# Kernel optimization log

Hardware: AMD Instinct MI355X
Metric: run time of the kernel (lower is better)

## Reference

```python
import jax, jax.numpy as jnp
import numpy as np

D_MODEL = 1024
N_HEADS = 16
D_K = D_MODEL // N_HEADS

def _xavier(key, shape):
    fan_in, fan_out = shape[1], shape[0]
    limit = float(np.sqrt(6.0 / (fan_in + fan_out)))
    return jax.random.uniform(key, shape, jnp.float32, -limit, limit)

def setup_inputs() -> dict:
    key = jax.random.key(0)
    ks = jax.random.split(key, 7)
    B, S = 2, 2048
    return {
        "query": jax.random.normal(ks[0], (B, S, D_MODEL), jnp.float32),
        "key": jax.random.normal(ks[1], (B, S, D_MODEL), jnp.float32),
        "value": jax.random.normal(ks[2], (B, S, D_MODEL), jnp.float32),
        "w_q": _xavier(ks[3], (D_MODEL, D_MODEL)),  # torch Linear weight [out, in]
        "w_k": _xavier(ks[4], (D_MODEL, D_MODEL)),
        "w_v": _xavier(ks[5], (D_MODEL, D_MODEL)),
        "w_o": _xavier(ks[6], (D_MODEL, D_MODEL)),
        "ln_gamma": jnp.ones((D_MODEL,), jnp.float32),
        "ln_beta": jnp.zeros((D_MODEL,), jnp.float32),
    }

def reference(query, key, value, w_q, w_k, w_v, w_o, ln_gamma, ln_beta):
    B, S, _ = query.shape
    # projections (torch Linear: x @ W.T), split into heads -> [B, H, S, d_k]
    def split_heads(x, W):
        return (x @ W.T).reshape(B, S, N_HEADS, D_K).transpose(0, 2, 1, 3)
    Q = split_heads(query, w_q)
    K = split_heads(key, w_k)
    V = split_heads(value, w_v)
    scores = jnp.einsum('bhqd,bhkd->bhqk', Q, K) / jnp.sqrt(jnp.float32(D_K))
    attn = jax.nn.softmax(scores, axis=-1)  # dropout disabled (p=0 / eval)
    ctx = jnp.einsum('bhqk,bhkd->bhqd', attn, V)
    ctx = ctx.transpose(0, 2, 1, 3).reshape(B, S, D_MODEL)
    out = ctx @ w_o.T
    # residual + LayerNorm
    x = query + out
    mu = jnp.mean(x, axis=-1, keepdims=True)
    var = jnp.var(x, axis=-1, keepdims=True)
    return (x - mu) / jnp.sqrt(var + 1e-5) * ln_gamma + ln_beta
```

## Files before the change

### kernel.cpp

```cpp
#include <hip/hip_runtime.h>
#include <hip/hip_bf16.h>

#define DEVI __device__ __forceinline__

typedef float f32x4 __attribute__((ext_vector_type(4)));
typedef short bf16x8 __attribute__((ext_vector_type(8)));
typedef unsigned short ushort_t;

DEVI ushort_t f2bf(float x) {
  union { float f; unsigned u; } c; c.f = x;
  unsigned u = c.u;
  unsigned r = (u + 0x7fffu + ((u >> 16) & 1u)) >> 16;
  return (ushort_t)r;
}

DEVI float bf2f(unsigned hw) {
  union { unsigned u; float f; } c; c.u = hw << 16; return c.f;
}

DEVI unsigned cvt_pk_bf16(float lo, float hi) {
  unsigned r;
  asm volatile("v_cvt_pk_bf16_f32 %0, %1, %2" : "=v"(r) : "v"(lo), "v"(hi));
  return r;
}

DEVI void gload16(const ushort_t* g, ushort_t* l) {
  __builtin_amdgcn_global_load_lds(
      (const __attribute__((address_space(1))) unsigned int*)g,
      (__attribute__((address_space(3))) unsigned int*)l, 16, 0, 0);
}

#define WAITL0() asm volatile("s_waitcnt lgkmcnt(0)" ::: "memory")


__global__ __launch_bounds__(256)
void cvt_all_kernel(const float* __restrict__ p0, const float* __restrict__ p1,
                    const float* __restrict__ p2,
                    const float* __restrict__ w0, const float* __restrict__ w1,
                    const float* __restrict__ w2, const float* __restrict__ w3,
                    ushort_t* __restrict__ o0, ushort_t* __restrict__ o1,
                    ushort_t* __restrict__ o2,
                    ushort_t* __restrict__ q0, ushort_t* __restrict__ q1,
                    ushort_t* __restrict__ q2, ushort_t* __restrict__ q3) {
  int z = blockIdx.y;
  int i = blockIdx.x * 256 + threadIdx.x;
  const float* in;
  ushort_t* out;
  if (z < 3) {
    in = (z == 0) ? p0 : (z == 1) ? p1 : p2;
    out = (z == 0) ? o0 : (z == 1) ? o1 : o2;
  } else {
    int w = i >> 17;
    int local = i & 131071;
    in = ((w == 0) ? w0 : (w == 1) ? w1 : (w == 2) ? w2 : w3);
    out = ((w == 0) ? q0 : (w == 1) ? q1 : (w == 2) ? q2 : q3);
    i = local;
  }
  const float4* p = (const float4*)in + (size_t)i * 2;
  float4 a = p[0], b = p[1];
  uint4 v;
  v.x = cvt_pk_bf16(a.x, a.y);
  v.y = cvt_pk_bf16(a.z, a.w);
  v.z = cvt_pk_bf16(b.x, b.y);
  v.w = cvt_pk_bf16(b.z, b.w);
  ((uint4*)out)[i] = v;
}


__global__ __launch_bounds__(256)
void gemm128(const ushort_t* __restrict__ A0, const ushort_t* __restrict__ A1,
             const ushort_t* __restrict__ A2,
             const ushort_t* __restrict__ W0, const ushort_t* __restrict__ W1,
             const ushort_t* __restrict__ W2,
             void* __restrict__ O0, void* __restrict__ O1,
             void* __restrict__ O2, int mode_base, int nsteps, float qscale) {
  constexpr int K = 1024;
  int z = blockIdx.z;
  int mode = (mode_base == 3) ? 3 : mode_base + z;
  const ushort_t* A = (z == 0) ? A0 : (z == 1) ? A1 : A2;
  const ushort_t* W = (z == 0) ? W0 : (z == 1) ? W1 : W2;
  void* Op = (z == 0) ? O0 : (z == 1) ? O1 : O2;
  if (mode == 3) {
    A = A0 + z * 512;
    W = W0 + z * 512;
    Op = z ? O1 : O0;
  }
  float scale = (mode == 0) ? qscale : 1.0f;
  int m0 = (mode == 2) ? blockIdx.x * 128 : blockIdx.y * 128;
  int n0 = (mode == 2) ? blockIdx.y * 128 : blockIdx.x * 128;

  __shared__ __align__(16) ushort_t Asm[2][128 * 64];
  __shared__ __align__(16) ushort_t Bsm[2][128 * 64];

  int t = threadIdx.x;
  int lane = t & 63, wave = t >> 6;
  int wm = wave >> 1, wn = wave & 1;
  int col = lane & 15, g = lane >> 4;
  int lr = lane >> 3, lc = lane & 7;
  int cswz = col & 7;

  const ushort_t* aSrc = A + (size_t)(m0 + wave * 32 + lr) * K + (lc ^ lr) * 8;
  const ushort_t* bSrc = W + (size_t)(n0 + wave * 32 + lr) * K + (lc ^ lr) * 8;

  f32x4 z4 = {0.f, 0.f, 0.f, 0.f};
  f32x4 acc[4][4];
  for (int i = 0; i < 4; i++)
    for (int j = 0; j < 4; j++) acc[i][j] = z4;

#define GEMM_STAGE(buf, koff) do {                                         \
    _Pragma("unroll")                                                      \
    for (int i_ = 0; i_ < 4; i_++) {                                       \
      gload16(aSrc + (koff) + i_ * 8 * K,                                  \
              &Asm[buf][(wave * 32 + i_ * 8) * 64]);                       \
      gload16(bSrc + (koff) + i_ * 8 * K,                                  \
              &Bsm[buf][(wave * 32 + i_ * 8) * 64]);                       \
    }                                                                      \
  } while (0)

  GEMM_STAGE(0, 0);
  __syncthreads();

  for (int kt = 0; kt < nsteps; ++kt) {
    int cur = kt & 1;
    if (kt < nsteps - 1) GEMM_STAGE(cur ^ 1, (kt + 1) * 64);
    const ushort_t* As = Asm[cur];
    const ushort_t* Bs = Bsm[cur];
#pragma unroll
    for (int kk = 0; kk < 2; ++kk) {
      bf16x8 af[4], bfr[4];
#pragma unroll
      for (int mi = 0; mi < 4; mi++) {
        int row = wm * 64 + mi * 16 + col;
        af[mi] = *(const bf16x8*)(As + row * 64 + (((kk * 4 + g) ^ cswz) * 8));
      }
#pragma unroll
      for (int ni = 0; ni < 4; ni++) {
        int row = wn * 64 + ni * 16 + col;
        bfr[ni] = *(const bf16x8*)(Bs + row * 64 + (((kk * 4 + g) ^ cswz) * 8));
      }
      __builtin_amdgcn_s_setprio(1);
#pragma unroll
      for (int mi = 0; mi < 4; mi++)
#pragma unroll
        for (int ni = 0; ni < 4; ni++)
          acc[mi][ni] = __builtin_amdgcn_mfma_f32_16x16x32_bf16(af[mi], bfr[ni],
                                                                acc[mi][ni], 0, 0, 0);
      __builtin_amdgcn_s_setprio(0);
    }
    __syncthreads();
  }

#pragma unroll
  for (int mi = 0; mi < 4; mi++)
#pragma unroll
    for (int ni = 0; ni < 4; ni++)
#pragma unroll
      for (int r = 0; r < 4; r++) {
        int m = m0 + wm * 64 + mi * 16 + g * 4 + r;
        int n = n0 + wn * 64 + ni * 16 + col;
        float v = acc[mi][ni][r] * scale;
        if (mode <= 1) {
          int b = m >> 11, s = m & 2047, h = n >> 6, d = n & 63;
          ((ushort_t*)Op)[(((size_t)(b * 16 + h) * 2048 + s) * 64) + d] = f2bf(v);
        } else if (mode == 2) {
          int h = m >> 6, d = m & 63, b = n >> 11, s = n & 2047;
          ((ushort_t*)Op)[(((size_t)(b * 16 + h) * 64 + d) * 2048) + s] = f2bf(v);
        } else {
          ((ushort_t*)Op)[(size_t)m * 1024 + n] = f2bf(v);
        }
      }
#undef GEMM_STAGE
}


__global__ __launch_bounds__(256, 4)
void attn_kernel(const ushort_t* __restrict__ Qh, const ushort_t* __restrict__ Kh,
                 const ushort_t* __restrict__ Vt,
                 ushort_t* __restrict__ op0, ushort_t* __restrict__ op1,
                 float* __restrict__ lp0, float* __restrict__ lp1) {
  int qt = blockIdx.x;
  int bh = blockIdx.y;
  int sp = blockIdx.z;
  int t = threadIdx.x, lane = t & 63, wave = t >> 6;
  int col = lane & 15, g = lane >> 4;
  int lr = lane >> 3, lc = lane & 7;
  int cswz = col & 7;
  int q0 = qt * 128 + wave * 32;
  int kbase = sp * 1024;
  ushort_t* opart = sp ? op1 : op0;
  float* lpart = sp ? lp1 : lp0;

  const ushort_t* Qp = Qh + (size_t)bh * 2048 * 64;
  const ushort_t* Kp = Kh + (size_t)bh * 2048 * 64;
  const ushort_t* Vp = Vt + (size_t)bh * 64 * 2048;

  __shared__ __align__(16) ushort_t Ksm[2][64 * 64];
  __shared__ __align__(16) ushort_t Vsm[2][64 * 64];

  int slot0 = wave * 16 + lr;
  int slot1 = slot0 + 8;
  int key0 = (slot0 & 0x20) | ((slot0 & 0x0C) << 1) | ((slot0 & 0x10) >> 2) | (slot0 & 3);
  int key1 = (slot1 & 0x20) | ((slot1 & 0x0C) << 1) | ((slot1 & 0x10) >> 2) | (slot1 & 3);

  const ushort_t* kSrc0 = Kp + (size_t)key0 * 64 + (lc ^ lr) * 8;
  const ushort_t* kSrc1 = Kp + (size_t)key1 * 64 + (lc ^ lr) * 8;
  const ushort_t* vSrc = Vp + (size_t)(wave * 16 + lr) * 2048 + (lc ^ lr) * 8;

#define ATTN_STAGE(buf, k0) do { \
    gload16(kSrc0 + (size_t)(k0) * 64, &Ksm[buf][wave * 1024]);        \
    gload16(kSrc1 + (size_t)(k0) * 64, &Ksm[buf][wave * 1024 + 512]);  \
    gload16(vSrc + (k0),               &Vsm[buf][wave * 1024]);        \
    gload16(vSrc + (k0) + 16384,       &Vsm[buf][wave * 1024 + 512]);  \
  } while (0)

  bf16x8 qa0 = *(const bf16x8*)(Qp + (size_t)(q0 + col) * 64 + g * 8);
  bf16x8 qa1 = *(const bf16x8*)(Qp + (size_t)(q0 + col) * 64 + 32 + g * 8);
  bf16x8 qb0 = *(const bf16x8*)(Qp + (size_t)(q0 + 16 + col) * 64 + g * 8);
  bf16x8 qb1 = *(const bf16x8*)(Qp + (size_t)(q0 + 16 + col) * 64 + 32 + g * 8);

  f32x4 z4 = {0.f, 0.f, 0.f, 0.f};
  f32x4 oa[4], ob[4];
  for (int i = 0; i < 4; i++) { oa[i] = z4; ob[i] = z4; }
  f32x4 la = z4, lb = z4;

  ATTN_STAGE(0, kbase);
  __syncthreads();

  for (int it = 0; it < 16; ++it) {
    int cur = it & 1;
    int k0 = kbase + it * 64;
    if (it < 15) ATTN_STAGE(cur ^ 1, k0 + 64);

    const ushort_t* Ks = Ksm[cur];
    const ushort_t* Vs = Vsm[cur];

    f32x4 sa[4], sb[4];
#pragma unroll
    for (int kt = 0; kt < 4; kt++) {
      int off = (kt * 16 + col) * 64 + ((g ^ cswz) * 8);
      bf16x8 kf0 = *(const bf16x8*)(Ks + off);
      bf16x8 kf1 = *(const bf16x8*)(Ks + (off ^ 32));
      f32x4 a = z4, b = z4;
      __builtin_amdgcn_s_setprio(1);
      a = __builtin_amdgcn_mfma_f32_16x16x32_bf16(kf0, qa0, a, 0, 0, 0);
      a = __builtin_amdgcn_mfma_f32_16x16x32_bf16(kf1, qa1, a, 0, 0, 0);
      b = __builtin_amdgcn_mfma_f32_16x16x32_bf16(kf0, qb0, b, 0, 0, 0);
      b = __builtin_amdgcn_mfma_f32_16x16x32_bf16(kf1, qb1, b, 0, 0, 0);
      __builtin_amdgcn_s_setprio(0);
      sa[kt] = a; sb[kt] = b;
    }

    unsigned pka[8], pkb[8];
#pragma unroll
    for (int kt = 0; kt < 4; kt++) {
      float a0 = __builtin_amdgcn_exp2f(sa[kt][0]);
      float a1 = __builtin_amdgcn_exp2f(sa[kt][1]);
      float a2 = __builtin_amdgcn_exp2f(sa[kt][2]);
      float a3 = __builtin_amdgcn_exp2f(sa[kt][3]);
      la[0] += a0; la[1] += a1; la[2] += a2; la[3] += a3;
      pka[2 * kt]     = cvt_pk_bf16(a0, a1);
      pka[2 * kt + 1] = cvt_pk_bf16(a2, a3);
      float b0 = __builtin_amdgcn_exp2f(sb[kt][0]);
      float b1 = __builtin_amdgcn_exp2f(sb[kt][1]);
      float b2 = __builtin_amdgcn_exp2f(sb[kt][2]);
      float b3 = __builtin_amdgcn_exp2f(sb[kt][3]);
      lb[0] += b0; lb[1] += b1; lb[2] += b2; lb[3] += b3;
      pkb[2 * kt]     = cvt_pk_bf16(b0, b1);
      pkb[2 * kt + 1] = cvt_pk_bf16(b2, b3);
    }

#pragma unroll
    for (int kk = 0; kk < 2; kk++) {
      union { uint4 u; bf16x8 f; } ua, ub;
      ua.u.x = pka[4 * kk];     ua.u.y = pka[4 * kk + 1];
      ua.u.z = pka[4 * kk + 2]; ua.u.w = pka[4 * kk + 3];
      ub.u.x = pkb[4 * kk];     ub.u.y = pkb[4 * kk + 1];
      ub.u.z = pkb[4 * kk + 2]; ub.u.w = pkb[4 * kk + 3];
      __builtin_amdgcn_s_setprio(1);
#pragma unroll
      for (int dt = 0; dt < 4; dt++) {
        bf16x8 vf = *(const bf16x8*)(Vs + (dt * 16 + col) * 64 +
                                     (((kk * 4 + g) ^ cswz) * 8));
        oa[dt] = __builtin_amdgcn_mfma_f32_16x16x32_bf16(vf, ua.f, oa[dt], 0, 0, 0);
        ob[dt] = __builtin_amdgcn_mfma_f32_16x16x32_bf16(vf, ub.f, ob[dt], 0, 0, 0);
      }
      __builtin_amdgcn_s_setprio(0);
    }
    __syncthreads();
  }
#undef ATTN_STAGE

  float lva = (la[0] + la[1]) + (la[2] + la[3]);
  lva += __shfl_xor(lva, 16);
  lva += __shfl_xor(lva, 32);
  float lvb = (lb[0] + lb[1]) + (lb[2] + lb[3]);
  lvb += __shfl_xor(lvb, 16);
  lvb += __shfl_xor(lvb, 32);
  if (g == 0) {
    lpart[(size_t)bh * 2048 + q0 + col] = lva;
    lpart[(size_t)bh * 2048 + q0 + 16 + col] = lvb;
  }
  int b = bh >> 4, h = bh & 15;
#pragma unroll
  for (int dt = 0; dt < 4; dt++)
#pragma unroll
    for (int r = 0; r < 4; r++) {
      int d = dt * 16 + g * 4 + r;
      opart[((size_t)(b * 2048 + q0 + col)) * 1024 + h * 64 + d] =
          f2bf(oa[dt][r]);
      opart[((size_t)(b * 2048 + q0 + 16 + col)) * 1024 + h * 64 + d] =
          f2bf(ob[dt][r]);
    }
}


__global__ __launch_bounds__(256)
void attn_reduce(const ushort_t* __restrict__ o0, const ushort_t* __restrict__ o1,
                 const float* __restrict__ l0, const float* __restrict__ l1,
                 ushort_t* __restrict__ ctx) {
  int m = blockIdx.x;
  int t = threadIdx.x;
  int b = m >> 11, q = m & 2047;
  int h = t >> 4;
  size_t li = (size_t)(b * 16 + h) * 2048 + q;
  float inv = 1.0f / (l0[li] + l1[li]);
  uint2 a = ((const uint2*)(o0 + (size_t)m * 1024))[t];
  uint2 c = ((const uint2*)(o1 + (size_t)m * 1024))[t];
  float x0 = (bf2f(a.x & 0xffffu) + bf2f(c.x & 0xffffu)) * inv;
  float x1 = (bf2f(a.x >> 16)     + bf2f(c.x >> 16))     * inv;
  float x2 = (bf2f(a.y & 0xffffu) + bf2f(c.y & 0xffffu)) * inv;
  float x3 = (bf2f(a.y >> 16)     + bf2f(c.y >> 16))     * inv;
  uint2 o;
  o.x = cvt_pk_bf16(x0, x1);
  o.y = cvt_pk_bf16(x2, x3);
  ((uint2*)(ctx + (size_t)m * 1024))[t] = o;
}


__global__ __launch_bounds__(256)
void ln_kernel(const float* __restrict__ resid, const ushort_t* __restrict__ p0,
               const ushort_t* __restrict__ p1,
               const float* __restrict__ gamma, const float* __restrict__ beta,
               float* __restrict__ out) {
  int m = blockIdx.x;
  int t = threadIdx.x;
  int lane = t & 63, wave = t >> 6;
  float4 a = ((const float4*)(resid + (size_t)m * 1024))[t];
  uint2 v0 = ((const uint2*)(p0 + (size_t)m * 1024))[t];
  uint2 v1 = ((const uint2*)(p1 + (size_t)m * 1024))[t];
  float4 x;
  x.x = a.x + bf2f(v0.x & 0xffffu) + bf2f(v1.x & 0xffffu);
  x.y = a.y + bf2f(v0.x >> 16)     + bf2f(v1.x >> 16);
  x.z = a.z + bf2f(v0.y & 0xffffu) + bf2f(v1.y & 0xffffu);
  x.w = a.w + bf2f(v0.y >> 16)     + bf2f(v1.y >> 16);
  float sum = (x.x + x.y) + (x.z + x.w);
  float ssq = x.x * x.x + x.y * x.y + x.z * x.z + x.w * x.w;
  for (int off = 1; off < 64; off <<= 1) {
    sum += __shfl_xor(sum, off);
    ssq += __shfl_xor(ssq, off);
  }
  __shared__ float red[8];
  if (lane == 0) { red[wave] = sum; red[4 + wave] = ssq; }
  __syncthreads();
  sum = red[0] + red[1] + red[2] + red[3];
  ssq = red[4] + red[5] + red[6] + red[7];
  float mu = sum * (1.f / 1024.f);
  float var = ssq * (1.f / 1024.f) - mu * mu;
  float rstd = rsqrtf(var + 1e-5f);
  const float4* gp = (const float4*)gamma;
  const float4* bp = (const float4*)beta;
  float4 gg = gp[t], bb = bp[t];
  float4 y;
  y.x = (x.x - mu) * rstd * gg.x + bb.x;
  y.y = (x.y - mu) * rstd * gg.y + bb.y;
  y.z = (x.z - mu) * rstd * gg.z + bb.z;
  y.w = (x.w - mu) * rstd * gg.w + bb.w;
  ((float4*)(out + (size_t)m * 1024))[t] = y;
}


extern "C" void kernel_launch(void* const* d_in, const int* in_sizes, int n_in,
                              void* d_out, int out_size, void* d_ws, size_t ws_size,
                              hipStream_t stream) {
  (void)in_sizes; (void)n_in; (void)out_size; (void)ws_size;
  const float* query = (const float*)d_in[0];
  const float* keyi  = (const float*)d_in[1];
  const float* value = (const float*)d_in[2];
  const float* w_q = (const float*)d_in[3];
  const float* w_k = (const float*)d_in[4];
  const float* w_v = (const float*)d_in[5];
  const float* w_o = (const float*)d_in[6];
  const float* ln_g = (const float*)d_in[7];
  const float* ln_b = (const float*)d_in[8];

  char* ws = (char*)d_ws;
  const size_t MB = 1u << 20;
  ushort_t* Xq  = (ushort_t*)(ws + 0 * MB);
  ushort_t* Xk  = (ushort_t*)(ws + 8 * MB);
  ushort_t* Xv  = (ushort_t*)(ws + 16 * MB);
  ushort_t* op0 = (ushort_t*)(ws + 0 * MB);
  ushort_t* op1 = (ushort_t*)(ws + 8 * MB);
  float*    l0  = (float*)   (ws + 16 * MB);
  float*    l1  = (float*)   (ws + 17 * MB);
  ushort_t* proj0 = (ushort_t*)(ws + 0 * MB);
  ushort_t* proj1 = (ushort_t*)(ws + 8 * MB);
  ushort_t* Wq  = (ushort_t*)(ws + 24 * MB);
  ushort_t* Wk  = (ushort_t*)(ws + 26 * MB);
  ushort_t* Wv  = (ushort_t*)(ws + 28 * MB);
  ushort_t* Wo  = (ushort_t*)(ws + 30 * MB);
  ushort_t* Qh  = (ushort_t*)(ws + 32 * MB);
  ushort_t* Kh  = (ushort_t*)(ws + 40 * MB);
  ushort_t* Vt  = (ushort_t*)(ws + 48 * MB);
  ushort_t* ctx = (ushort_t*)(ws + 56 * MB);

  const float SCL = 0.18033688f;

  cvt_all_kernel<<<dim3(2048, 4), 256, 0, stream>>>(
      query, keyi, value, w_q, w_k, w_v, w_o,
      Xq, Xk, Xv, Wq, Wk, Wv, Wo);

  gemm128<<<dim3(8, 32, 3), 256, 0, stream>>>(Xq, Xk, Wv, Wq, Wk, Xv,
                                              Qh, Kh, Vt, 0, 16, SCL);
  attn_kernel<<<dim3(16, 32, 2), 256, 0, stream>>>(Qh, Kh, Vt,
                                                   op0, op1, l0, l1);
  attn_reduce<<<4096, 256, 0, stream>>>(op0, op1, l0, l1, ctx);
  gemm128<<<dim3(8, 32, 2), 256, 0, stream>>>(ctx, ctx, ctx, Wo, Wo, Wo,
                                              proj0, proj1, proj0, 3, 8, 1.0f);
  ln_kernel<<<4096, 256, 0, stream>>>(query, proj0, proj1, ln_g, ln_b,
                                      (float*)d_out);
}
```

Baseline: 140.8 us.

## Single-buffer GEMM LDS tiles and swap grid axes for tile rasterization

The projection GEMM drops its double-buffered LDS prefetch. Each k-step now loads its tile, synchronizes, then computes, which halves shared memory per block so more blocks can be resident. The launch grid is also transposed, so consecutive blocks walk along the M (token) dimension instead of N, which changes L2 reuse of the weight and activation tiles. The cost is that global-to-LDS loads no longer overlap with the MFMA work inside a block, and the kernel now relies on other resident blocks to hide that latency.

```diff
diff --git a/kernel.cpp b/kernel.cpp
--- a/kernel.cpp
+++ b/kernel.cpp
@@ -86,11 +86,11 @@
     Op = z ? O1 : O0;
   }
   float scale = (mode == 0) ? qscale : 1.0f;
-  int m0 = (mode == 2) ? blockIdx.x * 128 : blockIdx.y * 128;
-  int n0 = (mode == 2) ? blockIdx.y * 128 : blockIdx.x * 128;
-
-  __shared__ __align__(16) ushort_t Asm[2][128 * 64];
-  __shared__ __align__(16) ushort_t Bsm[2][128 * 64];
+  int m0 = (mode == 2) ? blockIdx.y * 128 : blockIdx.x * 128;
+  int n0 = (mode == 2) ? blockIdx.x * 128 : blockIdx.y * 128;
+
+  __shared__ __align__(16) ushort_t Asm[128 * 64];
+  __shared__ __align__(16) ushort_t Bsm[128 * 64];
 
   int t = threadIdx.x;
   int lane = t & 63, wave = t >> 6;
@@ -107,36 +107,26 @@
   for (int i = 0; i < 4; i++)
     for (int j = 0; j < 4; j++) acc[i][j] = z4;
 
-#define GEMM_STAGE(buf, koff) do {                                         \
-    _Pragma("unroll")                                                      \
-    for (int i_ = 0; i_ < 4; i_++) {                                       \
-      gload16(aSrc + (koff) + i_ * 8 * K,                                  \
-              &Asm[buf][(wave * 32 + i_ * 8) * 64]);                       \
-      gload16(bSrc + (koff) + i_ * 8 * K,                                  \
-              &Bsm[buf][(wave * 32 + i_ * 8) * 64]);                       \
-    }                                                                      \
-  } while (0)
-
-  GEMM_STAGE(0, 0);
-  __syncthreads();
-
   for (int kt = 0; kt < nsteps; ++kt) {
-    int cur = kt & 1;
-    if (kt < nsteps - 1) GEMM_STAGE(cur ^ 1, (kt + 1) * 64);
-    const ushort_t* As = Asm[cur];
-    const ushort_t* Bs = Bsm[cur];
+    int koff = kt * 64;
+#pragma unroll
+    for (int i_ = 0; i_ < 4; i_++) {
+      gload16(aSrc + koff + i_ * 8 * K, &Asm[(wave * 32 + i_ * 8) * 64]);
+      gload16(bSrc + koff + i_ * 8 * K, &Bsm[(wave * 32 + i_ * 8) * 64]);
+    }
+    __syncthreads();
 #pragma unroll
     for (int kk = 0; kk < 2; ++kk) {
       bf16x8 af[4], bfr[4];
 #pragma unroll
       for (int mi = 0; mi < 4; mi++) {
         int row = wm * 64 + mi * 16 + col;
-        af[mi] = *(const bf16x8*)(As + row * 64 + (((kk * 4 + g) ^ cswz) * 8));
+        af[mi] = *(const bf16x8*)(Asm + row * 64 + (((kk * 4 + g) ^ cswz) * 8));
       }
 #pragma unroll
       for (int ni = 0; ni < 4; ni++) {
         int row = wn * 64 + ni * 16 + col;
-        bfr[ni] = *(const bf16x8*)(Bs + row * 64 + (((kk * 4 + g) ^ cswz) * 8));
+        bfr[ni] = *(const bf16x8*)(Bsm + row * 64 + (((kk * 4 + g) ^ cswz) * 8));
       }
       __builtin_amdgcn_s_setprio(1);
 #pragma unroll
@@ -169,7 +159,6 @@
           ((ushort_t*)Op)[(size_t)m * 1024 + n] = f2bf(v);
         }
       }
-#undef GEMM_STAGE
 }
 
 
@@ -419,12 +408,12 @@
       query, keyi, value, w_q, w_k, w_v, w_o,
       Xq, Xk, Xv, Wq, Wk, Wv, Wo);
 
-  gemm128<<<dim3(8, 32, 3), 256, 0, stream>>>(Xq, Xk, Wv, Wq, Wk, Xv,
+  gemm128<<<dim3(32, 8, 3), 256, 0, stream>>>(Xq, Xk, Wv, Wq, Wk, Xv,
                                               Qh, Kh, Vt, 0, 16, SCL);
   attn_kernel<<<dim3(16, 32, 2), 256, 0, stream>>>(Qh, Kh, Vt,
                                                    op0, op1, l0, l1);
   attn_reduce<<<4096, 256, 0, stream>>>(op0, op1, l0, l1, ctx);
-  gemm128<<<dim3(8, 32, 2), 256, 0, stream>>>(ctx, ctx, ctx, Wo, Wo, Wo,
+  gemm128<<<dim3(32, 8, 2), 256, 0, stream>>>(ctx, ctx, ctx, Wo, Wo, Wo,
                                               proj0, proj1, proj0, 3, 8, 1.0f);
   ln_kernel<<<4096, 256, 0, stream>>>(query, proj0, proj1, ln_g, ln_b,
                                       (float*)d_out);
```

Measured after the change: 127.3 us. -9.6%, faster.
